# Performance work log

Measured on AMD Instinct MI355X. Metric: run time of the kernel, lower is better.

Reference implementation:

```python
import jax, jax.numpy as jnp
import numpy as np

PARTIAL_DATA_THRESHOLD = 0.1  # threshold on squared NN distance (ChamferDistance returns squared dists)


def setup_inputs() -> dict:
    key = jax.random.key(0)
    k1, k2 = jax.random.split(key)
    scan_vertices = jax.random.normal(k1, (50000, 3), dtype=jnp.float32)      # N x 3
    template_vertices = jax.random.normal(k2, (6890, 3), dtype=jnp.float32)   # M x 3
    return {"scan_vertices": scan_vertices, "template_vertices": template_vertices}


def reference(scan_vertices, template_vertices):
    # Directional (template -> scan) Chamfer: for each template point, squared
    # distance to nearest scan point; then sum distances below threshold.
    # d2[m, n] = |t_m|^2 + |s_n|^2 - 2 t_m . s_n
    t_sq = jnp.sum(template_vertices * template_vertices, axis=-1)            # [M]
    s_sq = jnp.sum(scan_vertices * scan_vertices, axis=-1)                    # [N]
    cross = jnp.einsum('md,nd->mn', template_vertices, scan_vertices)         # [M, N]
    d2 = t_sq[:, None] + s_sq[None, :] - 2.0 * cross                          # [M, N]
    template2scan = jnp.min(d2, axis=1)                                       # [M]
    mask = template2scan < PARTIAL_DATA_THRESHOLD
    return jnp.sum(jnp.where(mask, template2scan, 0.0))
```

## Files before the change

### kernel.cpp

```cpp
#include <hip/hip_runtime.h>
#include <hip/hip_bf16.h>

#define BLK 256
#define SPLITS 25
#define FPS 64
#define FRTOT (SPLITS * FPS)
#define NSLOT (FRTOT * 32)
#define THRESH 0.1f
#define KEY_MAX 0xFFFFFFFFu
#define ONE_BF ((unsigned short)0x3F80)

typedef __attribute__((ext_vector_type(8))) short short8;
typedef __attribute__((ext_vector_type(16))) float floatx16;

__device__ __forceinline__ unsigned short f2bf(float x) {
    unsigned u = __float_as_uint(x);
    unsigned r = u + 0x7FFFu + ((u >> 16) & 1u);
    return (unsigned short)(r >> 16);
}
__device__ __forceinline__ float bf2f(unsigned short h) {
    return __uint_as_float(((unsigned)h) << 16);
}

__device__ __forceinline__ unsigned f2key(float f) {
    unsigned b = __float_as_uint(f);
    return (b & 0x80000000u) ? ~b : (b | 0x80000000u);
}
__device__ __forceinline__ float key2f(unsigned k) {
    return __uint_as_float((k & 0x80000000u) ? (k & 0x7FFFFFFFu) : ~k);
}

template <int CTRL>
__device__ __forceinline__ float dpp_ror_min(float v) {
    const int i = __float_as_int(v);
    const int p = __builtin_amdgcn_update_dpp(i, i, CTRL, 0xF, 0xF, false);
    return fminf(v, __int_as_float(p));
}

__global__ __launch_bounds__(BLK) void pdl_prep(const float* __restrict__ scan,
                                                uint4* __restrict__ fragbuf,
                                                unsigned* __restrict__ gmin,
                                                float* __restrict__ out,
                                                int N, int Mpad) {
    const int n = blockIdx.x * BLK + threadIdx.x;
    if (n == 0) out[0] = 0.0f;
    if (n < Mpad) gmin[n] = KEY_MAX;
    if (n >= NSLOT) return;

    unsigned short k[16];
    if (n < N) {
        const float x = scan[3 * n + 0], y = scan[3 * n + 1], z = scan[3 * n + 2];
        const float s2 = fmaf(x, x, fmaf(y, y, z * z));
        const float cx = -2.0f * x, cy = -2.0f * y, cz = -2.0f * z;
        const unsigned short xh = f2bf(cx); const unsigned short xl = f2bf(cx - bf2f(xh));
        const unsigned short yh = f2bf(cy); const unsigned short yl = f2bf(cy - bf2f(yh));
        const unsigned short zh = f2bf(cz); const unsigned short zl = f2bf(cz - bf2f(zh));
        const unsigned short wh = f2bf(s2); const unsigned short wl = f2bf(s2 - bf2f(wh));
        k[0] = xh; k[1] = xl; k[2] = xh; k[3] = xl;
        k[4] = yh; k[5] = yl; k[6] = yh; k[7] = yl;
        k[8] = zh; k[9] = zl; k[10] = zh; k[11] = zl;
        k[12] = ONE_BF; k[13] = ONE_BF;
        k[14] = wh; k[15] = wl;
    } else {
#pragma unroll
        for (int i = 0; i < 16; ++i) k[i] = 0;
        k[12] = ONE_BF; k[13] = ONE_BF;
        k[14] = f2bf(1e30f); k[15] = 0;
    }

    const int g = n >> 5, c = n & 31;
    uint4 lo, hi;
    lo.x = (unsigned)k[0] | ((unsigned)k[1] << 16);
    lo.y = (unsigned)k[2] | ((unsigned)k[3] << 16);
    lo.z = (unsigned)k[4] | ((unsigned)k[5] << 16);
    lo.w = (unsigned)k[6] | ((unsigned)k[7] << 16);
    hi.x = (unsigned)k[8] | ((unsigned)k[9] << 16);
    hi.y = (unsigned)k[10] | ((unsigned)k[11] << 16);
    hi.z = (unsigned)k[12] | ((unsigned)k[13] << 16);
    hi.w = (unsigned)k[14] | ((unsigned)k[15] << 16);
    fragbuf[(size_t)g * 64 + c] = lo;
    fragbuf[(size_t)g * 64 + 32 + c] = hi;
}

__global__ __launch_bounds__(BLK, 2) void pdl_main(const float* __restrict__ tmpl,
                                                   const uint4* __restrict__ fragbuf,
                                                   unsigned* __restrict__ gmin,
                                                   int M) {
    const int tid = threadIdx.x;
    const int wave = tid >> 6, lane = tid & 63;

    const int mbase = (blockIdx.y * 4 + wave) * 64;
    short8 A0, A1;
#pragma unroll
    for (int af = 0; af < 2; ++af) {
        int m = mbase + af * 32 + (lane & 31);
        if (m > M - 1) m = M - 1;
        const float x = tmpl[3 * m + 0], y = tmpl[3 * m + 1], z = tmpl[3 * m + 2];
        const float t2 = fmaf(x, x, fmaf(y, y, z * z));
        const unsigned short xh = f2bf(x); const unsigned short xl = f2bf(x - bf2f(xh));
        const unsigned short yh = f2bf(y); const unsigned short yl = f2bf(y - bf2f(yh));
        const unsigned short zh = f2bf(z); const unsigned short zl = f2bf(z - bf2f(zh));
        const unsigned short wh = f2bf(t2); const unsigned short wl = f2bf(t2 - bf2f(wh));
        const bool hi = (lane >= 32);
        short8 a;
        a[0] = (short)(hi ? zh : xh);
        a[1] = (short)(hi ? zh : xh);
        a[2] = (short)(hi ? zl : xl);
        a[3] = (short)(hi ? zl : xl);
        a[4] = (short)(hi ? wh : yh);
        a[5] = (short)(hi ? wl : yh);
        a[6] = (short)(hi ? ONE_BF : yl);
        a[7] = (short)(hi ? ONE_BF : yl);
        if (af == 0) A0 = a; else A1 = a;
    }

    floatx16 mn0, mn1, zacc;
#pragma unroll
    for (int r = 0; r < 16; ++r) { mn0[r] = 3e30f; mn1[r] = 3e30f; zacc[r] = 0.0f; }

    const uint4* fb = fragbuf + (size_t)(blockIdx.x * FPS) * 64 + lane;

    union U { uint4 u; short8 s; };
    uint4 p0 = fb[0 * 64], p1 = fb[1 * 64];
#pragma unroll 1
    for (int f = 0; f < FPS; f += 2) {
        U c0, c1;
        c0.u = p0; c1.u = p1;
        p0 = fb[(size_t)(f + 2) * 64];
        p1 = fb[(size_t)(f + 3) * 64];
        const floatx16 d00 = __builtin_amdgcn_mfma_f32_32x32x16_bf16(A0, c0.s, zacc, 0, 0, 0);
        const floatx16 d10 = __builtin_amdgcn_mfma_f32_32x32x16_bf16(A1, c0.s, zacc, 0, 0, 0);
        const floatx16 d01 = __builtin_amdgcn_mfma_f32_32x32x16_bf16(A0, c1.s, zacc, 0, 0, 0);
        const floatx16 d11 = __builtin_amdgcn_mfma_f32_32x32x16_bf16(A1, c1.s, zacc, 0, 0, 0);
#pragma unroll
        for (int r = 0; r < 16; ++r) {
            mn0[r] = fminf(fminf(d00[r], d01[r]), mn0[r]);
            mn1[r] = fminf(fminf(d10[r], d11[r]), mn1[r]);
        }
    }

#pragma unroll
    for (int af = 0; af < 2; ++af) {
#pragma unroll
        for (int r = 0; r < 16; ++r) {
            float v = (af == 0) ? mn0[r] : mn1[r];
            v = dpp_ror_min<0x128>(v);
            v = dpp_ror_min<0x124>(v);
            v = dpp_ror_min<0x122>(v);
            v = dpp_ror_min<0x121>(v);
            const int sw = __builtin_amdgcn_ds_swizzle(__float_as_int(v), 0x401F);
            v = fminf(v, __int_as_float(sw));
            if ((lane & 31) == 0) {
                const int row = (r & 3) + 8 * (r >> 2) + ((lane >> 5) << 2);
                atomicMin(&gmin[mbase + af * 32 + row], f2key(v));
            }
        }
    }
}

__global__ __launch_bounds__(BLK) void pdl_final(const unsigned* __restrict__ gmin,
                                                 float* __restrict__ out, int M) {
    const int m = blockIdx.x * BLK + threadIdx.x;
    float s = 0.0f;
    if (m < M) {
        const float v = key2f(gmin[m]);
        if (v < THRESH) s = v;
    }
#pragma unroll
    for (int off = 32; off > 0; off >>= 1) s += __shfl_down(s, off, 64);

    __shared__ float ls[BLK / 64];
    const int lane = threadIdx.x & 63;
    const int w = threadIdx.x >> 6;
    if (lane == 0) ls[w] = s;
    __syncthreads();
    if (threadIdx.x == 0) {
        float t = 0.0f;
#pragma unroll
        for (int i = 0; i < BLK / 64; ++i) t += ls[i];
        atomicAdd(out, t);
    }
}

extern "C" void kernel_launch(void* const* d_in, const int* in_sizes, int n_in,
                              void* d_out, int out_size, void* d_ws, size_t ws_size,
                              hipStream_t stream) {
    const float* scan = (const float*)d_in[0];
    const float* tmpl = (const float*)d_in[1];
    float* out = (float*)d_out;

    const int N = in_sizes[0] / 3;
    const int M = in_sizes[1] / 3;

    const int tGroups = (M + 255) / 256;
    const int Mpad = tGroups * 256;

    unsigned* gmin = (unsigned*)d_ws;
    uint4* fragbuf = (uint4*)((char*)d_ws + 65536);

    pdl_prep<<<(NSLOT + BLK - 1) / BLK, BLK, 0, stream>>>(scan, fragbuf, gmin,
                                                          out, N, Mpad);

    dim3 grid(SPLITS, tGroups);
    pdl_main<<<grid, BLK, 0, stream>>>(tmpl, fragbuf, gmin, M);

    pdl_final<<<(M + BLK - 1) / BLK, BLK, 0, stream>>>(gmin, out, M);
}
```

Baseline: 81.24 us.

## Switch distance MFMA from 32x32x16 to 16x16x32 tiles with smaller wave tiles

Replaces the 32x32x16 bf16 MFMA with 16x16x32 bf16 MFMA, packing each point's split-bf16 coordinates into a 32-wide K dimension where half the K lanes are zero. The scan fragment layout, template tiling (32 templates per wave), split count, frames per split and occupancy bound are changed to match, and the prefetch depth rises to four fragments. The intent is smaller accumulators, fewer registers, higher occupancy and more blocks (more template groups). The cost is that half of each MFMA's K work is wasted on zero padding.

New measurement: 86.04 us. +5.9%, slower.

```diff
diff --git a/kernel.cpp b/kernel.cpp
--- a/kernel.cpp
+++ b/kernel.cpp
@@ -2,16 +2,16 @@
 #include <hip/hip_bf16.h>
 
 #define BLK 256
-#define SPLITS 25
-#define FPS 64
+#define SPLITS 24
+#define FPS 136
 #define FRTOT (SPLITS * FPS)
-#define NSLOT (FRTOT * 32)
+#define NSLOT (FRTOT * 16)
 #define THRESH 0.1f
 #define KEY_MAX 0xFFFFFFFFu
 #define ONE_BF ((unsigned short)0x3F80)
 
 typedef __attribute__((ext_vector_type(8))) short short8;
-typedef __attribute__((ext_vector_type(16))) float floatx16;
+typedef __attribute__((ext_vector_type(4))) float floatx4;
 
 __device__ __forceinline__ unsigned short f2bf(float x) {
     unsigned u = __float_as_uint(x);
@@ -68,7 +68,7 @@
         k[14] = f2bf(1e30f); k[15] = 0;
     }
 
-    const int g = n >> 5, c = n & 31;
+    const int g = n >> 4, c = n & 15;
     uint4 lo, hi;
     lo.x = (unsigned)k[0] | ((unsigned)k[1] << 16);
     lo.y = (unsigned)k[2] | ((unsigned)k[3] << 16);
@@ -78,22 +78,23 @@
     hi.y = (unsigned)k[10] | ((unsigned)k[11] << 16);
     hi.z = (unsigned)k[12] | ((unsigned)k[13] << 16);
     hi.w = (unsigned)k[14] | ((unsigned)k[15] << 16);
-    fragbuf[(size_t)g * 64 + c] = lo;
-    fragbuf[(size_t)g * 64 + 32 + c] = hi;
-}
-
-__global__ __launch_bounds__(BLK, 2) void pdl_main(const float* __restrict__ tmpl,
+    fragbuf[(size_t)g * 32 + c] = lo;
+    fragbuf[(size_t)g * 32 + 16 + c] = hi;
+}
+
+__global__ __launch_bounds__(BLK, 6) void pdl_main(const float* __restrict__ tmpl,
                                                    const uint4* __restrict__ fragbuf,
                                                    unsigned* __restrict__ gmin,
                                                    int M) {
     const int tid = threadIdx.x;
     const int wave = tid >> 6, lane = tid & 63;
-
-    const int mbase = (blockIdx.y * 4 + wave) * 64;
+    const int quad = lane >> 4, col = lane & 15;
+
+    const int mbase = (blockIdx.y * 4 + wave) * 32;
     short8 A0, A1;
 #pragma unroll
     for (int af = 0; af < 2; ++af) {
-        int m = mbase + af * 32 + (lane & 31);
+        int m = mbase + af * 16 + col;
         if (m > M - 1) m = M - 1;
         const float x = tmpl[3 * m + 0], y = tmpl[3 * m + 1], z = tmpl[3 * m + 2];
         const float t2 = fmaf(x, x, fmaf(y, y, z * z));
@@ -101,58 +102,67 @@
         const unsigned short yh = f2bf(y); const unsigned short yl = f2bf(y - bf2f(yh));
         const unsigned short zh = f2bf(z); const unsigned short zl = f2bf(z - bf2f(zh));
         const unsigned short wh = f2bf(t2); const unsigned short wl = f2bf(t2 - bf2f(wh));
-        const bool hi = (lane >= 32);
+        const bool q0 = (quad == 0), q1 = (quad == 1);
         short8 a;
-        a[0] = (short)(hi ? zh : xh);
-        a[1] = (short)(hi ? zh : xh);
-        a[2] = (short)(hi ? zl : xl);
-        a[3] = (short)(hi ? zl : xl);
-        a[4] = (short)(hi ? wh : yh);
-        a[5] = (short)(hi ? wl : yh);
-        a[6] = (short)(hi ? ONE_BF : yl);
-        a[7] = (short)(hi ? ONE_BF : yl);
+        a[0] = (short)(q0 ? xh : (q1 ? zh : 0));
+        a[1] = (short)(q0 ? xh : (q1 ? zh : 0));
+        a[2] = (short)(q0 ? xl : (q1 ? zl : 0));
+        a[3] = (short)(q0 ? xl : (q1 ? zl : 0));
+        a[4] = (short)(q0 ? yh : (q1 ? wh : 0));
+        a[5] = (short)(q0 ? yh : (q1 ? wl : 0));
+        a[6] = (short)(q0 ? yl : (q1 ? ONE_BF : 0));
+        a[7] = (short)(q0 ? yl : (q1 ? ONE_BF : 0));
         if (af == 0) A0 = a; else A1 = a;
     }
 
-    floatx16 mn0, mn1, zacc;
-#pragma unroll
-    for (int r = 0; r < 16; ++r) { mn0[r] = 3e30f; mn1[r] = 3e30f; zacc[r] = 0.0f; }
-
-    const uint4* fb = fragbuf + (size_t)(blockIdx.x * FPS) * 64 + lane;
+    floatx4 mn0, mn1, zacc;
+#pragma unroll
+    for (int r = 0; r < 4; ++r) { mn0[r] = 3e30f; mn1[r] = 3e30f; zacc[r] = 0.0f; }
+
+    const uint4* fb = fragbuf + (size_t)(blockIdx.x * FPS) * 32 + (lane & 31);
 
     union U { uint4 u; short8 s; };
-    uint4 p0 = fb[0 * 64], p1 = fb[1 * 64];
+    uint4 p0 = fb[0 * 32], p1 = fb[1 * 32], p2 = fb[2 * 32], p3 = fb[3 * 32];
 #pragma unroll 1
-    for (int f = 0; f < FPS; f += 2) {
-        U c0, c1;
-        c0.u = p0; c1.u = p1;
-        p0 = fb[(size_t)(f + 2) * 64];
-        p1 = fb[(size_t)(f + 3) * 64];
-        const floatx16 d00 = __builtin_amdgcn_mfma_f32_32x32x16_bf16(A0, c0.s, zacc, 0, 0, 0);
-        const floatx16 d10 = __builtin_amdgcn_mfma_f32_32x32x16_bf16(A1, c0.s, zacc, 0, 0, 0);
-        const floatx16 d01 = __builtin_amdgcn_mfma_f32_32x32x16_bf16(A0, c1.s, zacc, 0, 0, 0);
-        const floatx16 d11 = __builtin_amdgcn_mfma_f32_32x32x16_bf16(A1, c1.s, zacc, 0, 0, 0);
-#pragma unroll
-        for (int r = 0; r < 16; ++r) {
+    for (int f = 0; f < FPS; f += 4) {
+        U c0, c1, c2, c3;
+        c0.u = p0; c1.u = p1; c2.u = p2; c3.u = p3;
+        p0 = fb[(size_t)(f + 4) * 32];
+        p1 = fb[(size_t)(f + 5) * 32];
+        p2 = fb[(size_t)(f + 6) * 32];
+        p3 = fb[(size_t)(f + 7) * 32];
+        const floatx4 d00 = __builtin_amdgcn_mfma_f32_16x16x32_bf16(A0, c0.s, zacc, 0, 0, 0);
+        const floatx4 d10 = __builtin_amdgcn_mfma_f32_16x16x32_bf16(A1, c0.s, zacc, 0, 0, 0);
+        const floatx4 d01 = __builtin_amdgcn_mfma_f32_16x16x32_bf16(A0, c1.s, zacc, 0, 0, 0);
+        const floatx4 d11 = __builtin_amdgcn_mfma_f32_16x16x32_bf16(A1, c1.s, zacc, 0, 0, 0);
+#pragma unroll
+        for (int r = 0; r < 4; ++r) {
             mn0[r] = fminf(fminf(d00[r], d01[r]), mn0[r]);
             mn1[r] = fminf(fminf(d10[r], d11[r]), mn1[r]);
         }
+        const floatx4 d02 = __builtin_amdgcn_mfma_f32_16x16x32_bf16(A0, c2.s, zacc, 0, 0, 0);
+        const floatx4 d12 = __builtin_amdgcn_mfma_f32_16x16x32_bf16(A1, c2.s, zacc, 0, 0, 0);
+        const floatx4 d03 = __builtin_amdgcn_mfma_f32_16x16x32_bf16(A0, c3.s, zacc, 0, 0, 0);
+        const floatx4 d13 = __builtin_amdgcn_mfma_f32_16x16x32_bf16(A1, c3.s, zacc, 0, 0, 0);
+#pragma unroll
+        for (int r = 0; r < 4; ++r) {
+            mn0[r] = fminf(fminf(d02[r], d03[r]), mn0[r]);
+            mn1[r] = fminf(fminf(d12[r], d13[r]), mn1[r]);
+        }
     }
 
 #pragma unroll
     for (int af = 0; af < 2; ++af) {
 #pragma unroll
-        for (int r = 0; r < 16; ++r) {
+        for (int r = 0; r < 4; ++r) {
             float v = (af == 0) ? mn0[r] : mn1[r];
             v = dpp_ror_min<0x128>(v);
             v = dpp_ror_min<0x124>(v);
             v = dpp_ror_min<0x122>(v);
             v = dpp_ror_min<0x121>(v);
-            const int sw = __builtin_amdgcn_ds_swizzle(__float_as_int(v), 0x401F);
-            v = fminf(v, __int_as_float(sw));
-            if ((lane & 31) == 0) {
-                const int row = (r & 3) + 8 * (r >> 2) + ((lane >> 5) << 2);
-                atomicMin(&gmin[mbase + af * 32 + row], f2key(v));
+            if (col == 0) {
+                const int m = mbase + af * 16 + quad * 4 + r;
+                atomicMin(&gmin[m], f2key(v));
             }
         }
     }
@@ -192,8 +202,8 @@
     const int N = in_sizes[0] / 3;
     const int M = in_sizes[1] / 3;
 
-    const int tGroups = (M + 255) / 256;
-    const int Mpad = tGroups * 256;
+    const int tGroups = (M + 127) / 128;
+    const int Mpad = tGroups * 128;
 
     unsigned* gmin = (unsigned*)d_ws;
     uint4* fragbuf = (uint4*)((char*)d_ws + 65536);
```
